# Performance work log

Measured on AMD Instinct MI355X. Metric: run time of the kernel, lower is better.

The kernel has to match this reference:

```python
import jax, jax.numpy as jnp
import numpy as np

EPS = 1e-7  # tf.keras.backend.epsilon()
DEGREE = 5
SCALE_BASE = 1.0
SCALE_LEGENDRE = 1.0


def legendre_basis(x, degree):
    # min/max normalization over the feature axis -> x_norm in [-1, 1]
    x_min = jnp.min(x, axis=-1, keepdims=True)
    x_max = jnp.max(x, axis=-1, keepdims=True)
    x_norm = 2.0 * (x - x_min) / (x_max - x_min + EPS) - 1.0
    polys = [jnp.ones_like(x_norm), x_norm]
    for n in range(2, degree + 1):
        p_n = ((2 * n - 1) * x_norm * polys[-1] - (n - 1) * polys[-2]) / n
        polys.append(p_n)
    return jnp.stack(polys, axis=-1)  # [b, i, degree+1]


def setup_inputs() -> dict:
    key = jax.random.key(0)
    k1, k2, k3 = jax.random.split(key, 3)
    b, i, o, d = 4096, 1024, 1024, DEGREE + 1
    x = jax.random.normal(k1, (b, i), dtype=jnp.float32)
    # HeUniform: limit = sqrt(6 / fan_in)
    lim_b = np.sqrt(6.0 / i)
    base_weight = jax.random.uniform(k2, (i, o), dtype=jnp.float32, minval=-lim_b, maxval=lim_b)
    legendre_weight = jax.random.uniform(k3, (i, o, d), dtype=jnp.float32, minval=-lim_b, maxval=lim_b)
    return {"x": x, "base_weight": base_weight, "legendre_weight": legendre_weight}


def reference(x, base_weight, legendre_weight):
    base_output = jax.nn.silu(x @ base_weight)  # [b, o]
    basis = legendre_basis(x, DEGREE)  # [b, i, d]
    # 'bi,iod,bid->bo' == fold x into the basis then contract (i, d)
    xb = x[..., None] * basis  # [b, i, d]
    legendre_output = jnp.einsum('bid,iod->bo', xb, legendre_weight)
    return SCALE_BASE * base_output + SCALE_LEGENDRE * legendre_output
```

## Files before the change

### kernel.cpp

```cpp
#include <hip/hip_runtime.h>
#include <stdint.h>

typedef unsigned short u16;
typedef unsigned int   u32;
typedef __attribute__((ext_vector_type(8)))  short bhalf8;
typedef __attribute__((ext_vector_type(16))) float f32x16;

#define B_ROWS 4096
#define I_DIM  1024
#define O_DIM  1024
#define N_D    6
#define K_LEG  (I_DIM * N_D)

#define BM 256
#define BN 256
#define BK 64
#define NS 28
#define BUF_BYTES 65536
#define LDS_BYTES 131072

__device__ __forceinline__ u16 f2b(float f) {
  u32 u = __float_as_uint(f);
  return (u16)((u + 0x7fffu + ((u >> 16) & 1u)) >> 16);
}

__device__ __forceinline__ void gld_lds16(const void* g, void* l) {
  __builtin_amdgcn_global_load_lds(
      (const __attribute__((address_space(1))) u32*)(uintptr_t)g,
      (__attribute__((address_space(3))) u32*)(u32)(uintptr_t)l, 16, 0, 0);
}

#define RS 201
__global__ void k_prep(const float* __restrict__ bw, const float* __restrict__ lw,
                       const float* __restrict__ x,
                       u16* __restrict__ Bb, u16* __restrict__ Bl,
                       u16* __restrict__ Ab, u16* __restrict__ Al) {
  __shared__ float t[32 * RS];
  if (blockIdx.x < 1024) {
    const int bx = blockIdx.x & 31, by = blockIdx.x >> 5;
    const int i0 = by * 32, o0 = bx * 32;
    const int c = threadIdx.x & 31, r0 = threadIdx.x >> 5;
    #pragma unroll
    for (int k = 0; k < 4; ++k) {
      int r = r0 + k * 8;
      t[r * 33 + c] = bw[(size_t)(i0 + r) * O_DIM + o0 + c];
    }
    __syncthreads();
    #pragma unroll
    for (int k = 0; k < 4; ++k) {
      int r = r0 + k * 8;
      Bb[(size_t)(o0 + r) * I_DIM + i0 + c] = f2b(t[c * 33 + r]);
    }
  } else if (blockIdx.x < 2048) {
    const int blk = blockIdx.x - 1024;
    const int bx = blk & 31, by = blk >> 5;
    const int i0 = by * 32, o0 = bx * 32;
    for (int q = threadIdx.x; q < 32 * 48; q += 256) {
      int ri = q / 48, s4 = q % 48;
      float4 v = *(const float4*)(lw + (size_t)(i0 + ri) * (O_DIM * N_D) + o0 * N_D + s4 * 4);
      float* p = t + ri * RS + s4 * 4;
      p[0] = v.x; p[1] = v.y; p[2] = v.z; p[3] = v.w;
    }
    __syncthreads();
    for (int q = threadIdx.x; q < 32 * 96; q += 256) {
      int ro = q / 96, k = q % 96;
      int e0 = 2 * k, e1 = 2 * k + 1;
      float v0 = t[(e0 / 6) * RS + ro * 6 + (e0 % 6)];
      float v1 = t[(e1 / 6) * RS + ro * 6 + (e1 % 6)];
      u32* dst = (u32*)(Bl + (size_t)(o0 + ro) * K_LEG + i0 * N_D);
      dst[k] = (u32)f2b(v0) | ((u32)f2b(v1) << 16);
    }
  } else {
    const int b = blockIdx.x - 2048;
    const int tt = threadIdx.x;
    float4 v = ((const float4*)(x + (size_t)b * I_DIM))[tt];
    float mn = fminf(fminf(v.x, v.y), fminf(v.z, v.w));
    float mx = fmaxf(fmaxf(v.x, v.y), fmaxf(v.z, v.w));
    #pragma unroll
    for (int off = 32; off > 0; off >>= 1) {
      mn = fminf(mn, __shfl_xor(mn, off, 64));
      mx = fmaxf(mx, __shfl_xor(mx, off, 64));
    }
    __shared__ float smn[4], smx[4];
    if ((tt & 63) == 0) { smn[tt >> 6] = mn; smx[tt >> 6] = mx; }
    __syncthreads();
    mn = fminf(fminf(smn[0], smn[1]), fminf(smn[2], smn[3]));
    mx = fmaxf(fmaxf(smx[0], smx[1]), fmaxf(smx[2], smx[3]));
    float sc = 2.0f / (mx - mn + 1e-7f);

    float xs[4] = {v.x, v.y, v.z, v.w};
    u32 lb[12];
    #pragma unroll
    for (int e = 0; e < 4; ++e) {
      float xv = xs[e];
      float xn = (xv - mn) * sc - 1.0f;
      float p0 = 1.0f, p1 = xn;
      float p2 = (3.0f * xn * p1 - 1.0f * p0) * (1.0f / 2.0f);
      float p3 = (5.0f * xn * p2 - 2.0f * p1) * (1.0f / 3.0f);
      float p4 = (7.0f * xn * p3 - 3.0f * p2) * (1.0f / 4.0f);
      float p5 = (9.0f * xn * p4 - 4.0f * p3) * (1.0f / 5.0f);
      lb[e * 3 + 0] = (u32)f2b(xv * p0) | ((u32)f2b(xv * p1) << 16);
      lb[e * 3 + 1] = (u32)f2b(xv * p2) | ((u32)f2b(xv * p3) << 16);
      lb[e * 3 + 2] = (u32)f2b(xv * p4) | ((u32)f2b(xv * p5) << 16);
    }
    u32 a0 = (u32)f2b(xs[0]) | ((u32)f2b(xs[1]) << 16);
    u32 a1 = (u32)f2b(xs[2]) | ((u32)f2b(xs[3]) << 16);
    *(uint2*)(Ab + (size_t)b * I_DIM + tt * 4) = make_uint2(a0, a1);
    uint4* dl = (uint4*)(Al + (size_t)b * K_LEG + tt * 24);
    dl[0] = make_uint4(lb[0], lb[1], lb[2], lb[3]);
    dl[1] = make_uint4(lb[4], lb[5], lb[6], lb[7]);
    dl[2] = make_uint4(lb[8], lb[9], lb[10], lb[11]);
  }
}

__global__ __launch_bounds__(512, 2) void k_gemm(
    const u16* __restrict__ Ab, const u16* __restrict__ Bb,
    const u16* __restrict__ Al, const u16* __restrict__ Bl,
    float* __restrict__ out, float* __restrict__ P) {
  extern __shared__ char lds[];

  const int tid  = threadIdx.x;
  const int wave = tid >> 6;
  const int lane = tid & 63;
  const int wm = wave >> 2;
  const int wn = wave & 3;
  const u32 lr = (u32)lane & 31;
  const u32 hi = (u32)lane >> 5;

  const int bid   = blockIdx.x;
  const int bx    = bid >> 4;
  const int by    = (bid >> 2) & 3;
  const int split = bid & 3;
  const size_t brow = (size_t)bx * BM;
  const size_t bcol = (size_t)by * BN;
  const bool s0 = (split == 0);
  const int legbase = s0 ? 0 : (12 + 28 * (split - 1));

  const int rt = tid >> 3;
  const u32 ct = (((u32)tid & 7) ^ ((u32)rt & 7)) * 8;

  auto stage_half = [&](int v, int h) {
    char* dst = lds + (size_t)(v & 1) * BUF_BYTES + ((h >= 2) ? 32768 : 0)
              + (size_t)(h & 1) * 16384 + (size_t)tid * 16;
    const size_t rbase = ((h < 2) ? brow : bcol) + (size_t)(h & 1) * 128 + (size_t)rt;
    const u16* src0;
    size_t rstep;
    if (s0 && v < 16) {
      const u16* M = (h < 2) ? Ab : Bb;
      src0 = M + rbase * I_DIM + (size_t)v * BK + ct;
      rstep = (size_t)64 * I_DIM;
    } else {
      const int lv = s0 ? (v - 16) : (legbase + v);
      const u16* M = (h < 2) ? Al : Bl;
      src0 = M + rbase * K_LEG + (size_t)lv * BK + ct;
      rstep = (size_t)64 * K_LEG;
    }
    gld_lds16(src0, dst);
    gld_lds16(src0 + rstep, dst + 8192);
  };

  const u32 c0off = (hi ^ ((u32)lane & 7)) * 16;
  const u32 abase = ((u32)wm * 128 + lr) * 128;
  const u32 bbase = 32768u + ((u32)wn * 64 + lr) * 128;

  f32x16 acc[4][2] = {};
  bhalf8 afa[4], bfa[2], afb[4], bfb[2];

#define READF(AF, BF, P_, KK) do {                                            \
    const u32 co_ = c0off ^ ((KK) << 5);                                      \
    BF[0] = *(const bhalf8*)((P_) + bbase + co_);                             \
    BF[1] = *(const bhalf8*)((P_) + bbase + 4096 + co_);                      \
    AF[0] = *(const bhalf8*)((P_) + abase + co_);                             \
    AF[1] = *(const bhalf8*)((P_) + abase + 4096 + co_);                      \
    AF[2] = *(const bhalf8*)((P_) + abase + 8192 + co_);                      \
    AF[3] = *(const bhalf8*)((P_) + abase + 12288 + co_);                     \
  } while (0)

#define MM(AF, BF) do {                                                       \
    __builtin_amdgcn_s_setprio(1);                                            \
    _Pragma("unroll")                                                         \
    for (int m = 0; m < 4; ++m)                                               \
      _Pragma("unroll")                                                       \
      for (int n = 0; n < 2; ++n)                                             \
        acc[m][n] = __builtin_amdgcn_mfma_f32_32x32x16_bf16(AF[m], BF[n], acc[m][n], 0, 0, 0); \
    __builtin_amdgcn_s_setprio(0);                                            \
  } while (0)

  stage_half(0, 0); stage_half(0, 1); stage_half(0, 2); stage_half(0, 3);
  __syncthreads();

  for (int u = 0; u < NS; ++u) {
    if (s0 && u == 16) {
      #pragma unroll
      for (int m = 0; m < 4; ++m)
        #pragma unroll
        for (int n = 0; n < 2; ++n)
          #pragma unroll
          for (int j = 0; j < 16; ++j) {
            float v = acc[m][n][j];
            acc[m][n][j] = v / (1.0f + __expf(-v));
          }
    }
    const char* p = lds + (size_t)(u & 1) * BUF_BYTES;
    const bool st = (u < NS - 1);
    READF(afa, bfa, p, 0);
    if (st) stage_half(u + 1, 0);
    READF(afb, bfb, p, 1);
    MM(afa, bfa);
    if (st) stage_half(u + 1, 1);
    READF(afa, bfa, p, 2);
    MM(afb, bfb);
    if (st) stage_half(u + 1, 2);
    READF(afb, bfb, p, 3);
    MM(afa, bfa);
    if (st) stage_half(u + 1, 3);
    MM(afb, bfb);
    __syncthreads();
  }
#undef READF
#undef MM

  float* dst = s0 ? out : (P + (size_t)(split - 1) * ((size_t)B_ROWS * O_DIM));
  #pragma unroll
  for (int m = 0; m < 4; ++m)
    #pragma unroll
    for (int n = 0; n < 2; ++n) {
      const size_t rb = brow + wm * 128 + m * 32 + 4 * hi;
      const size_t c  = bcol + wn * 64 + n * 32 + lr;
      #pragma unroll
      for (int j = 0; j < 16; ++j) {
        const size_t r = rb + (j & 3) + 8 * (j >> 2);
        dst[r * O_DIM + c] = acc[m][n][j];
      }
    }
}

__global__ void k_reduce(float* __restrict__ out, const float* __restrict__ P) {
  const size_t i = (size_t)blockIdx.x * 256 + threadIdx.x;
  const size_t NE = (size_t)B_ROWS * O_DIM / 4;
  float4 a = ((const float4*)out)[i];
  float4 b = ((const float4*)P)[i];
  float4 c = ((const float4*)P)[i + NE];
  float4 d = ((const float4*)P)[i + 2 * NE];
  a.x += b.x + c.x + d.x;  a.y += b.y + c.y + d.y;
  a.z += b.z + c.z + d.z;  a.w += b.w + c.w + d.w;
  ((float4*)out)[i] = a;
}

extern "C" void kernel_launch(void* const* d_in, const int* in_sizes, int n_in,
                              void* d_out, int out_size, void* d_ws, size_t ws_size,
                              hipStream_t stream) {
  const float* x  = (const float*)d_in[0];
  const float* bw = (const float*)d_in[1];
  const float* lw = (const float*)d_in[2];
  float* out = (float*)d_out;

  char* w = (char*)d_ws;
  u16*  Ab = (u16*)(w);
  u16*  Al = (u16*)(w + (size_t)8   * 1024 * 1024);
  u16*  Bb = (u16*)(w + (size_t)56  * 1024 * 1024);
  u16*  Bl = (u16*)(w + (size_t)58  * 1024 * 1024);
  float* P = (float*)(w + (size_t)72 * 1024 * 1024);

  hipFuncSetAttribute((const void*)k_gemm,
                      hipFuncAttributeMaxDynamicSharedMemorySize, LDS_BYTES);

  k_prep  <<<dim3(2048 + B_ROWS), 256, 0, stream>>>(bw, lw, x, Bb, Bl, Ab, Al);
  k_gemm  <<<dim3(4 * (B_ROWS / BM) * (O_DIM / BN)), 512, LDS_BYTES, stream>>>(Ab, Bb, Al, Bl, out, P);
  k_reduce<<<dim3((B_ROWS * O_DIM / 4) / 256), 256, 0, stream>>>(out, P);
}
```

Before: 108.5 us.

## Shrink GEMM tile to 128x128 with 2-way split-K and simplify reduction

Changes the fused GEMM block tile from 256x256 with 512 threads and 4-way split-K to 128x128 with 256 threads and 2-way split-K, doubling K steps per block. The staging uses incrementing global pointers and an explicit vmcnt wait plus barrier, and the reduce kernel now adds only one partial buffer. This cuts partial-sum traffic and the reduction cost, but it halves per-block operand reuse, raising global and L2 load volume per FLOP, and lengthens each block's serial K loop.

```diff
diff --git a/kernel.cpp b/kernel.cpp
--- a/kernel.cpp
+++ b/kernel.cpp
@@ -12,12 +12,12 @@
 #define N_D    6
 #define K_LEG  (I_DIM * N_D)
 
-#define BM 256
-#define BN 256
+#define BM 128
+#define BN 128
 #define BK 64
-#define NS 28
-#define BUF_BYTES 65536
-#define LDS_BYTES 131072
+#define NS 56
+#define BUF_BYTES 32768
+#define LDS_BYTES 65536
 
 __device__ __forceinline__ u16 f2b(float f) {
   u32 u = __float_as_uint(f);
@@ -113,7 +113,7 @@
   }
 }
 
-__global__ __launch_bounds__(512, 2) void k_gemm(
+__global__ __launch_bounds__(256, 2) void k_gemm(
     const u16* __restrict__ Ab, const u16* __restrict__ Bb,
     const u16* __restrict__ Al, const u16* __restrict__ Bl,
     float* __restrict__ out, float* __restrict__ P) {
@@ -122,49 +122,48 @@
   const int tid  = threadIdx.x;
   const int wave = tid >> 6;
   const int lane = tid & 63;
-  const int wm = wave >> 2;
-  const int wn = wave & 3;
+  const int wm = wave >> 1;
+  const int wn = wave & 1;
   const u32 lr = (u32)lane & 31;
   const u32 hi = (u32)lane >> 5;
 
   const int bid   = blockIdx.x;
   const int bx    = bid >> 4;
-  const int by    = (bid >> 2) & 3;
-  const int split = bid & 3;
+  const int by    = (bid >> 1) & 7;
+  const int split = bid & 1;
   const size_t brow = (size_t)bx * BM;
   const size_t bcol = (size_t)by * BN;
   const bool s0 = (split == 0);
-  const int legbase = s0 ? 0 : (12 + 28 * (split - 1));
+  const int legbase = s0 ? 0 : 40;
 
   const int rt = tid >> 3;
   const u32 ct = (((u32)tid & 7) ^ ((u32)rt & 7)) * 8;
 
-  auto stage_half = [&](int v, int h) {
-    char* dst = lds + (size_t)(v & 1) * BUF_BYTES + ((h >= 2) ? 32768 : 0)
-              + (size_t)(h & 1) * 16384 + (size_t)tid * 16;
-    const size_t rbase = ((h < 2) ? brow : bcol) + (size_t)(h & 1) * 128 + (size_t)rt;
-    const u16* src0;
-    size_t rstep;
-    if (s0 && v < 16) {
-      const u16* M = (h < 2) ? Ab : Bb;
-      src0 = M + rbase * I_DIM + (size_t)v * BK + ct;
-      rstep = (size_t)64 * I_DIM;
-    } else {
-      const int lv = s0 ? (v - 16) : (legbase + v);
-      const u16* M = (h < 2) ? Al : Bl;
-      src0 = M + rbase * K_LEG + (size_t)lv * BK + ct;
-      rstep = (size_t)64 * K_LEG;
-    }
-    gld_lds16(src0, dst);
-    gld_lds16(src0 + rstep, dst + 8192);
+  const u16 *gA, *gB;
+  size_t ldk, ldk32;
+  auto set_ptrs = [&](const u16* A, const u16* Bt, size_t ldk_, size_t kt) {
+    ldk = ldk_; ldk32 = 32 * ldk_;
+    gA = A  + (brow + rt) * ldk_ + kt * BK + ct;
+    gB = Bt + (bcol + rt) * ldk_ + kt * BK + ct;
   };
+  if (s0) set_ptrs(Ab, Bb, I_DIM, 0);
+  else    set_ptrs(Al, Bl, K_LEG, (size_t)legbase);
+
+  auto stg = [&](int v, int h) {
+    if (s0 && v == 16 && h == 0) set_ptrs(Al, Bl, K_LEG, 0);
+    char* dst = lds + (size_t)(v & 1) * BUF_BYTES + ((h >= 4) ? 16384 : 0)
+              + (size_t)(h & 3) * 4096 + (size_t)tid * 16;
+    const u16* src = ((h < 4) ? gA : gB) + (size_t)(h & 3) * ldk32;
+    gld_lds16(src, dst);
+    if (h == 7) { gA += BK; gB += BK; }
+  };
 
   const u32 c0off = (hi ^ ((u32)lane & 7)) * 16;
-  const u32 abase = ((u32)wm * 128 + lr) * 128;
-  const u32 bbase = 32768u + ((u32)wn * 64 + lr) * 128;
-
-  f32x16 acc[4][2] = {};
-  bhalf8 afa[4], bfa[2], afb[4], bfb[2];
+  const u32 abase = ((u32)wm * 64 + lr) * 128;
+  const u32 bbase = 16384u + ((u32)wn * 64 + lr) * 128;
+
+  f32x16 acc[2][2] = {};
+  bhalf8 fa0[2], fb0[2], fa1[2], fb1[2], fa2[2], fb2[2], fa3[2], fb3[2];
 
 #define READF(AF, BF, P_, KK) do {                                            \
     const u32 co_ = c0off ^ ((KK) << 5);                                      \
@@ -172,27 +171,26 @@
     BF[1] = *(const bhalf8*)((P_) + bbase + 4096 + co_);                      \
     AF[0] = *(const bhalf8*)((P_) + abase + co_);                             \
     AF[1] = *(const bhalf8*)((P_) + abase + 4096 + co_);                      \
-    AF[2] = *(const bhalf8*)((P_) + abase + 8192 + co_);                      \
-    AF[3] = *(const bhalf8*)((P_) + abase + 12288 + co_);                     \
   } while (0)
 
 #define MM(AF, BF) do {                                                       \
     __builtin_amdgcn_s_setprio(1);                                            \
     _Pragma("unroll")                                                         \
-    for (int m = 0; m < 4; ++m)                                               \
+    for (int m = 0; m < 2; ++m)                                               \
       _Pragma("unroll")                                                       \
       for (int n = 0; n < 2; ++n)                                             \
         acc[m][n] = __builtin_amdgcn_mfma_f32_32x32x16_bf16(AF[m], BF[n], acc[m][n], 0, 0, 0); \
     __builtin_amdgcn_s_setprio(0);                                            \
   } while (0)
 
-  stage_half(0, 0); stage_half(0, 1); stage_half(0, 2); stage_half(0, 3);
+  #pragma unroll
+  for (int h = 0; h < 8; ++h) stg(0, h);
   __syncthreads();
 
   for (int u = 0; u < NS; ++u) {
     if (s0 && u == 16) {
       #pragma unroll
-      for (int m = 0; m < 4; ++m)
+      for (int m = 0; m < 2; ++m)
         #pragma unroll
         for (int n = 0; n < 2; ++n)
           #pragma unroll
@@ -203,29 +201,31 @@
     }
     const char* p = lds + (size_t)(u & 1) * BUF_BYTES;
     const bool st = (u < NS - 1);
-    READF(afa, bfa, p, 0);
-    if (st) stage_half(u + 1, 0);
-    READF(afb, bfb, p, 1);
-    MM(afa, bfa);
-    if (st) stage_half(u + 1, 1);
-    READF(afa, bfa, p, 2);
-    MM(afb, bfb);
-    if (st) stage_half(u + 1, 2);
-    READF(afb, bfb, p, 3);
-    MM(afa, bfa);
-    if (st) stage_half(u + 1, 3);
-    MM(afb, bfb);
-    __syncthreads();
+    READF(fa0, fb0, p, 0);
+    if (st) { stg(u + 1, 0); stg(u + 1, 1); }
+    READF(fa1, fb1, p, 1);
+    MM(fa0, fb0);
+    if (st) { stg(u + 1, 2); stg(u + 1, 3); }
+    READF(fa2, fb2, p, 2);
+    MM(fa1, fb1);
+    if (st) { stg(u + 1, 4); stg(u + 1, 5); }
+    READF(fa3, fb3, p, 3);
+    MM(fa2, fb2);
+    if (st) { stg(u + 1, 6); stg(u + 1, 7); }
+    MM(fa3, fb3);
+    asm volatile("s_waitcnt vmcnt(0)" ::: "memory");
+    __builtin_amdgcn_s_barrier();
+    __builtin_amdgcn_sched_barrier(0);
   }
 #undef READF
 #undef MM
 
-  float* dst = s0 ? out : (P + (size_t)(split - 1) * ((size_t)B_ROWS * O_DIM));
+  float* dst = s0 ? out : P;
   #pragma unroll
-  for (int m = 0; m < 4; ++m)
+  for (int m = 0; m < 2; ++m)
     #pragma unroll
     for (int n = 0; n < 2; ++n) {
-      const size_t rb = brow + wm * 128 + m * 32 + 4 * hi;
+      const size_t rb = brow + wm * 64 + m * 32 + 4 * hi;
       const size_t c  = bcol + wn * 64 + n * 32 + lr;
       #pragma unroll
       for (int j = 0; j < 16; ++j) {
@@ -237,13 +237,9 @@
 
 __global__ void k_reduce(float* __restrict__ out, const float* __restrict__ P) {
   const size_t i = (size_t)blockIdx.x * 256 + threadIdx.x;
-  const size_t NE = (size_t)B_ROWS * O_DIM / 4;
   float4 a = ((const float4*)out)[i];
   float4 b = ((const float4*)P)[i];
-  float4 c = ((const float4*)P)[i + NE];
-  float4 d = ((const float4*)P)[i + 2 * NE];
-  a.x += b.x + c.x + d.x;  a.y += b.y + c.y + d.y;
-  a.z += b.z + c.z + d.z;  a.w += b.w + c.w + d.w;
+  a.x += b.x;  a.y += b.y;  a.z += b.z;  a.w += b.w;
   ((float4*)out)[i] = a;
 }
 
@@ -266,6 +262,6 @@
                       hipFuncAttributeMaxDynamicSharedMemorySize, LDS_BYTES);
 
   k_prep  <<<dim3(2048 + B_ROWS), 256, 0, stream>>>(bw, lw, x, Bb, Bl, Ab, Al);
-  k_gemm  <<<dim3(4 * (B_ROWS / BM) * (O_DIM / BN)), 512, LDS_BYTES, stream>>>(Ab, Bb, Al, Bl, out, P);
+  k_gemm  <<<dim3(2 * (B_ROWS / BM) * (O_DIM / BN)), 256, LDS_BYTES, stream>>>(Ab, Bb, Al, Bl, out, P);
   k_reduce<<<dim3((B_ROWS * O_DIM / 4) / 256), 256, 0, stream>>>(out, P);
 }
```

New measurement: 107.4 us. No clear change (-1.0%).

## Switch GEMM to 16x16x32 MFMA with 4-phase pipelined staging and bf16 split-K partials

Applied to the files above, without the earlier changes.

Rewrites the main GEMM loop to use 16x16x32 bf16 MFMAs with a new LDS layout and swizzle. Global-to-LDS loads are issued two stages ahead, and each iteration is split into four phases with explicit vmcnt/lgkmcnt waits, barriers and sched_barriers, so loads overlap with compute. Split-K partial sums are now stored as bf16 instead of fp32, which halves partial-buffer traffic in the gemm and reduce kernels. The cost is lower precision in the partials and fragile hand-tuned wait counts.

```diff
diff --git a/kernel.cpp b/kernel.cpp
--- a/kernel.cpp
+++ b/kernel.cpp
@@ -3,8 +3,8 @@
 
 typedef unsigned short u16;
 typedef unsigned int   u32;
-typedef __attribute__((ext_vector_type(8)))  short bhalf8;
-typedef __attribute__((ext_vector_type(16))) float f32x16;
+typedef __attribute__((ext_vector_type(8))) short bhalf8;
+typedef __attribute__((ext_vector_type(4))) float f32x4;
 
 #define B_ROWS 4096
 #define I_DIM  1024
@@ -12,16 +12,15 @@
 #define N_D    6
 #define K_LEG  (I_DIM * N_D)
 
-#define BM 256
-#define BN 256
-#define BK 64
-#define NS 28
-#define BUF_BYTES 65536
+#define NU 28
 #define LDS_BYTES 131072
 
 __device__ __forceinline__ u16 f2b(float f) {
   u32 u = __float_as_uint(f);
   return (u16)((u + 0x7fffu + ((u >> 16) & 1u)) >> 16);
+}
+__device__ __forceinline__ float b2f(u16 h) {
+  return __uint_as_float((u32)h << 16);
 }
 
 __device__ __forceinline__ void gld_lds16(const void* g, void* l) {
@@ -116,7 +115,7 @@
 __global__ __launch_bounds__(512, 2) void k_gemm(
     const u16* __restrict__ Ab, const u16* __restrict__ Bb,
     const u16* __restrict__ Al, const u16* __restrict__ Bl,
-    float* __restrict__ out, float* __restrict__ P) {
+    float* __restrict__ out, u16* __restrict__ Pb) {
   extern __shared__ char lds[];
 
   const int tid  = threadIdx.x;
@@ -124,126 +123,159 @@
   const int lane = tid & 63;
   const int wm = wave >> 2;
   const int wn = wave & 3;
-  const u32 lr = (u32)lane & 31;
-  const u32 hi = (u32)lane >> 5;
+  const u32 l15 = (u32)lane & 15;
 
   const int bid   = blockIdx.x;
   const int bx    = bid >> 4;
   const int by    = (bid >> 2) & 3;
   const int split = bid & 3;
-  const size_t brow = (size_t)bx * BM;
-  const size_t bcol = (size_t)by * BN;
+  const size_t brow = (size_t)bx * 256;
+  const size_t bcol = (size_t)by * 256;
   const bool s0 = (split == 0);
   const int legbase = s0 ? 0 : (12 + 28 * (split - 1));
 
-  const int rt = tid >> 3;
-  const u32 ct = (((u32)tid & 7) ^ ((u32)rt & 7)) * 8;
-
-  auto stage_half = [&](int v, int h) {
-    char* dst = lds + (size_t)(v & 1) * BUF_BYTES + ((h >= 2) ? 32768 : 0)
-              + (size_t)(h & 1) * 16384 + (size_t)tid * 16;
-    const size_t rbase = ((h < 2) ? brow : bcol) + (size_t)(h & 1) * 128 + (size_t)rt;
-    const u16* src0;
-    size_t rstep;
-    if (s0 && v < 16) {
-      const u16* M = (h < 2) ? Ab : Bb;
-      src0 = M + rbase * I_DIM + (size_t)v * BK + ct;
-      rstep = (size_t)64 * I_DIM;
-    } else {
-      const int lv = s0 ? (v - 16) : (legbase + v);
-      const u16* M = (h < 2) ? Al : Bl;
-      src0 = M + rbase * K_LEG + (size_t)lv * BK + ct;
-      rstep = (size_t)64 * K_LEG;
-    }
-    gld_lds16(src0, dst);
-    gld_lds16(src0 + rstep, dst + 8192);
+  const int rS = tid >> 2;
+  const u32 cS = (((u32)tid & 3) ^ (((u32)rS >> 1) & 3)) * 8;
+
+  auto stage = [&](int v, int h) {
+    const int isB = h & 1, kkh = h >> 1;
+    char* dst = lds + ((v & 1) * 65536 + isB * 32768 + kkh * 16384) + (size_t)tid * 16;
+    const u16* M; size_t ldk; int kt;
+    if (s0 && v < 16) { M = isB ? Bb : Ab; ldk = I_DIM; kt = v; }
+    else { M = isB ? Bl : Al; ldk = K_LEG; kt = s0 ? (v - 16) : (legbase + v); }
+    const u16* src = M + ((isB ? bcol : brow) + (size_t)rS) * ldk
+                   + (size_t)kt * 64 + kkh * 32 + cS;
+    gld_lds16(src, dst);
+    gld_lds16(src + 128 * ldk, dst + 8192);
   };
 
-  const u32 c0off = (hi ^ ((u32)lane & 7)) * 16;
-  const u32 abase = ((u32)wm * 128 + lr) * 128;
-  const u32 bbase = 32768u + ((u32)wn * 64 + lr) * 128;
-
-  f32x16 acc[4][2] = {};
-  bhalf8 afa[4], bfa[2], afb[4], bfb[2];
-
-#define READF(AF, BF, P_, KK) do {                                            \
-    const u32 co_ = c0off ^ ((KK) << 5);                                      \
-    BF[0] = *(const bhalf8*)((P_) + bbase + co_);                             \
-    BF[1] = *(const bhalf8*)((P_) + bbase + 4096 + co_);                      \
-    AF[0] = *(const bhalf8*)((P_) + abase + co_);                             \
-    AF[1] = *(const bhalf8*)((P_) + abase + 4096 + co_);                      \
-    AF[2] = *(const bhalf8*)((P_) + abase + 8192 + co_);                      \
-    AF[3] = *(const bhalf8*)((P_) + abase + 12288 + co_);                     \
-  } while (0)
-
-#define MM(AF, BF) do {                                                       \
+  const u32 chnk = ((((u32)lane >> 4) & 3) ^ ((l15 >> 1) & 3)) * 16;
+  const u32 aoff = ((u32)wm * 128 + l15) * 64 + chnk;
+  const u32 boff = 32768u + ((u32)wn * 64 + l15) * 64 + chnk;
+
+  f32x4 acc[8][4] = {};
+  bhalf8 Aev[8], Aod[8], Bn01[2], Bn23[2];
+
+  auto silu = [&]() {
+    #pragma unroll
+    for (int m = 0; m < 8; ++m)
+      #pragma unroll
+      for (int n = 0; n < 4; ++n)
+        #pragma unroll
+        for (int j = 0; j < 4; ++j) {
+          float v = acc[m][n][j];
+          acc[m][n][j] = v / (1.0f + __expf(-v));
+        }
+  };
+
+#define SB   __builtin_amdgcn_sched_barrier(0)
+#define BARR __builtin_amdgcn_s_barrier()
+#define VMW(N) asm volatile("s_waitcnt vmcnt(" #N ")" ::: "memory")
+#define RD_A(SET, DB, KKH) do { const char* q_ = lds + (DB) + (KKH)*16384 + aoff; \
+    SET[0]=*(const bhalf8*)(q_);      SET[1]=*(const bhalf8*)(q_+1024);       \
+    SET[2]=*(const bhalf8*)(q_+2048); SET[3]=*(const bhalf8*)(q_+3072);       \
+    SET[4]=*(const bhalf8*)(q_+4096); SET[5]=*(const bhalf8*)(q_+5120);       \
+    SET[6]=*(const bhalf8*)(q_+6144); SET[7]=*(const bhalf8*)(q_+7168); } while(0)
+#define RD_B01(DB, KKH) do { const char* q_ = lds + (DB) + (KKH)*16384 + boff; \
+    Bn01[0]=*(const bhalf8*)(q_);      Bn01[1]=*(const bhalf8*)(q_+1024); } while(0)
+#define RD_B23(DB, KKH) do { const char* q_ = lds + (DB) + (KKH)*16384 + boff; \
+    Bn23[0]=*(const bhalf8*)(q_+2048); Bn23[1]=*(const bhalf8*)(q_+3072); } while(0)
+#define MFMA8(ASET, B0_, B1_, NB) do {                                        \
     __builtin_amdgcn_s_setprio(1);                                            \
     _Pragma("unroll")                                                         \
-    for (int m = 0; m < 4; ++m)                                               \
-      _Pragma("unroll")                                                       \
-      for (int n = 0; n < 2; ++n)                                             \
-        acc[m][n] = __builtin_amdgcn_mfma_f32_32x32x16_bf16(AF[m], BF[n], acc[m][n], 0, 0, 0); \
+    for (int m_ = 0; m_ < 8; ++m_) {                                          \
+      acc[m_][NB]   = __builtin_amdgcn_mfma_f32_16x16x32_bf16(ASET[m_], B0_, acc[m_][NB],   0,0,0); \
+      acc[m_][NB+1] = __builtin_amdgcn_mfma_f32_16x16x32_bf16(ASET[m_], B1_, acc[m_][NB+1], 0,0,0); \
+    }                                                                         \
     __builtin_amdgcn_s_setprio(0);                                            \
-  } while (0)
-
-  stage_half(0, 0); stage_half(0, 1); stage_half(0, 2); stage_half(0, 3);
-  __syncthreads();
-
-  for (int u = 0; u < NS; ++u) {
-    if (s0 && u == 16) {
+  } while(0)
+
+#define PH1(DB, STG, WT) do { RD_B23(DB, 0); STG; SB; WT; BARR;               \
+    asm volatile("s_waitcnt lgkmcnt(2)" ::: "memory"); SB;                    \
+    MFMA8(Aev, Bn01[0], Bn01[1], 0); BARR; } while(0)
+#define PH2(DB, STG, WT) do { RD_A(Aod, DB, 1); RD_B01(DB, 1); STG; SB; WT; BARR; \
+    asm volatile("s_waitcnt lgkmcnt(10)" ::: "memory"); SB;                   \
+    MFMA8(Aev, Bn23[0], Bn23[1], 2); BARR; } while(0)
+#define PH3(DB, STG, WT) do { RD_B23(DB, 1); STG; SB; WT; BARR;               \
+    asm volatile("s_waitcnt lgkmcnt(2)" ::: "memory"); SB;                    \
+    MFMA8(Aod, Bn01[0], Bn01[1], 0); BARR; } while(0)
+#define PH4(DB2, STG) do { RD_A(Aev, DB2, 0); RD_B01(DB2, 0); STG; SB; BARR;  \
+    asm volatile("s_waitcnt lgkmcnt(10)" ::: "memory"); SB;                   \
+    MFMA8(Aod, Bn23[0], Bn23[1], 2); BARR; } while(0)
+#define PH4LAST() do {                                                        \
+    asm volatile("s_waitcnt lgkmcnt(0)" ::: "memory"); SB;                    \
+    MFMA8(Aod, Bn23[0], Bn23[1], 2); } while(0)
+
+  stage(0, 0); stage(0, 1); stage(0, 2); stage(0, 3);
+  stage(1, 0); stage(1, 1); stage(1, 2);
+  VMW(6); BARR;
+  RD_A(Aev, 0u, 0); RD_B01(0u, 0);
+
+  for (int u = 0; u < NU - 2; ++u) {
+    if (s0 && u == 16) silu();
+    const u32 db  = (u & 1) ? 65536u : 0u;
+    const u32 db2 = 65536u - db;
+    PH1(db, stage(u + 1, 3), VMW(10));
+    PH2(db, stage(u + 2, 0), VMW(10));
+    PH3(db, stage(u + 2, 1), VMW(8));
+    PH4(db2, stage(u + 2, 2));
+  }
+  PH1(0u, stage(27, 3), VMW(10));
+  PH2(0u, (void)0, VMW(8));
+  PH3(0u, (void)0, VMW(4));
+  PH4(65536u, (void)0);
+  PH1(65536u, (void)0, VMW(2));
+  PH2(65536u, (void)0, VMW(0));
+  PH3(65536u, (void)0, (void)0);
+  PH4LAST();
+
+#undef PH1
+#undef PH2
+#undef PH3
+#undef PH4
+#undef PH4LAST
+#undef MFMA8
+#undef RD_A
+#undef RD_B01
+#undef RD_B23
+
+  if (s0) {
+    #pragma unroll
+    for (int m = 0; m < 8; ++m)
       #pragma unroll
-      for (int m = 0; m < 4; ++m)
+      for (int n = 0; n < 4; ++n) {
+        const size_t r0 = brow + wm * 128 + m * 16 + (lane >> 4) * 4;
+        const size_t c  = bcol + wn * 64 + n * 16 + l15;
         #pragma unroll
-        for (int n = 0; n < 2; ++n)
-          #pragma unroll
-          for (int j = 0; j < 16; ++j) {
-            float v = acc[m][n][j];
-            acc[m][n][j] = v / (1.0f + __expf(-v));
-          }
-    }
-    const char* p = lds + (size_t)(u & 1) * BUF_BYTES;
-    const bool st = (u < NS - 1);
-    READF(afa, bfa, p, 0);
-    if (st) stage_half(u + 1, 0);
-    READF(afb, bfb, p, 1);
-    MM(afa, bfa);
-    if (st) stage_half(u + 1, 1);
-    READF(afa, bfa, p, 2);
-    MM(afb, bfb);
-    if (st) stage_half(u + 1, 2);
-    READF(afb, bfb, p, 3);
-    MM(afa, bfa);
-    if (st) stage_half(u + 1, 3);
-    MM(afb, bfb);
-    __syncthreads();
+        for (int j = 0; j < 4; ++j)
+          out[(r0 + j) * O_DIM + c] = acc[m][n][j];
+      }
+  } else {
+    u16* dst = Pb + (size_t)(split - 1) * ((size_t)B_ROWS * O_DIM);
+    #pragma unroll
+    for (int m = 0; m < 8; ++m)
+      #pragma unroll
+      for (int n = 0; n < 4; ++n) {
+        const size_t r0 = brow + wm * 128 + m * 16 + (lane >> 4) * 4;
+        const size_t c  = bcol + wn * 64 + n * 16 + l15;
+        #pragma unroll
+        for (int j = 0; j < 4; ++j)
+          dst[(r0 + j) * O_DIM + c] = f2b(acc[m][n][j]);
+      }
   }
-#undef READF
-#undef MM
-
-  float* dst = s0 ? out : (P + (size_t)(split - 1) * ((size_t)B_ROWS * O_DIM));
-  #pragma unroll
-  for (int m = 0; m < 4; ++m)
-    #pragma unroll
-    for (int n = 0; n < 2; ++n) {
-      const size_t rb = brow + wm * 128 + m * 32 + 4 * hi;
-      const size_t c  = bcol + wn * 64 + n * 32 + lr;
-      #pragma unroll
-      for (int j = 0; j < 16; ++j) {
-        const size_t r = rb + (j & 3) + 8 * (j >> 2);
-        dst[r * O_DIM + c] = acc[m][n][j];
-      }
-    }
-}
-
-__global__ void k_reduce(float* __restrict__ out, const float* __restrict__ P) {
+}
+
+__global__ void k_reduce(float* __restrict__ out, const u16* __restrict__ Pb) {
   const size_t i = (size_t)blockIdx.x * 256 + threadIdx.x;
-  const size_t NE = (size_t)B_ROWS * O_DIM / 4;
+  const size_t NE = (size_t)B_ROWS * O_DIM;
   float4 a = ((const float4*)out)[i];
-  float4 b = ((const float4*)P)[i];
-  float4 c = ((const float4*)P)[i + NE];
-  float4 d = ((const float4*)P)[i + 2 * NE];
-  a.x += b.x + c.x + d.x;  a.y += b.y + c.y + d.y;
-  a.z += b.z + c.z + d.z;  a.w += b.w + c.w + d.w;
+  ushort4 p0 = ((const ushort4*)Pb)[i];
+  ushort4 p1 = ((const ushort4*)(Pb + NE))[i];
+  ushort4 p2 = ((const ushort4*)(Pb + 2 * NE))[i];
+  a.x += b2f(p0.x) + b2f(p1.x) + b2f(p2.x);
+  a.y += b2f(p0.y) + b2f(p1.y) + b2f(p2.y);
+  a.z += b2f(p0.z) + b2f(p1.z) + b2f(p2.z);
+  a.w += b2f(p0.w) + b2f(p1.w) + b2f(p2.w);
   ((float4*)out)[i] = a;
 }
 
@@ -256,16 +288,16 @@
   float* out = (float*)d_out;
 
   char* w = (char*)d_ws;
-  u16*  Ab = (u16*)(w);
-  u16*  Al = (u16*)(w + (size_t)8   * 1024 * 1024);
-  u16*  Bb = (u16*)(w + (size_t)56  * 1024 * 1024);
-  u16*  Bl = (u16*)(w + (size_t)58  * 1024 * 1024);
-  float* P = (float*)(w + (size_t)72 * 1024 * 1024);
+  u16* Ab = (u16*)(w);
+  u16* Al = (u16*)(w + (size_t)8   * 1024 * 1024);
+  u16* Bb = (u16*)(w + (size_t)56  * 1024 * 1024);
+  u16* Bl = (u16*)(w + (size_t)58  * 1024 * 1024);
+  u16* Pb = (u16*)(w + (size_t)72  * 1024 * 1024);
 
   hipFuncSetAttribute((const void*)k_gemm,
                       hipFuncAttributeMaxDynamicSharedMemorySize, LDS_BYTES);
 
   k_prep  <<<dim3(2048 + B_ROWS), 256, 0, stream>>>(bw, lw, x, Bb, Bl, Ab, Al);
-  k_gemm  <<<dim3(4 * (B_ROWS / BM) * (O_DIM / BN)), 512, LDS_BYTES, stream>>>(Ab, Bb, Al, Bl, out, P);
-  k_reduce<<<dim3((B_ROWS * O_DIM / 4) / 256), 256, 0, stream>>>(out, P);
-}
+  k_gemm  <<<dim3(256), 512, LDS_BYTES, stream>>>(Ab, Bb, Al, Bl, out, Pb);
+  k_reduce<<<dim3((B_ROWS * O_DIM / 4) / 256), 256, 0, stream>>>(out, Pb);
+}
```

Measured after the change: 103.2 us. 1.05x faster.

## Store split-K partials as bf16 and restructure GEMM pipeline with staggered LDS reads

Applied to the files above, without the earlier changes.

Split-K partial results are now written as bf16 instead of fp32, halving partial write and reduce read traffic, with some accuracy loss in the partial sums. The main loop is rewritten into quarter steps with explicit lgkmcnt waits and sched_barriers around each MFMA batch. Waves in the two M halves read the K sub-chunks in a staggered order to spread LDS bank pressure. The loop now waits for vmcnt(0) plus a raw s_barrier instead of calling __syncthreads.

```diff
diff --git a/kernel.cpp b/kernel.cpp
--- a/kernel.cpp
+++ b/kernel.cpp
@@ -12,16 +12,15 @@
 #define N_D    6
 #define K_LEG  (I_DIM * N_D)
 
-#define BM 256
-#define BN 256
-#define BK 64
-#define NS 28
-#define BUF_BYTES 65536
+#define NU 28
 #define LDS_BYTES 131072
 
 __device__ __forceinline__ u16 f2b(float f) {
   u32 u = __float_as_uint(f);
   return (u16)((u + 0x7fffu + ((u >> 16) & 1u)) >> 16);
+}
+__device__ __forceinline__ float b2f(u16 h) {
+  return __uint_as_float((u32)h << 16);
 }
 
 __device__ __forceinline__ void gld_lds16(const void* g, void* l) {
@@ -116,7 +115,7 @@
 __global__ __launch_bounds__(512, 2) void k_gemm(
     const u16* __restrict__ Ab, const u16* __restrict__ Bb,
     const u16* __restrict__ Al, const u16* __restrict__ Bl,
-    float* __restrict__ out, float* __restrict__ P) {
+    float* __restrict__ out, u16* __restrict__ Pb) {
   extern __shared__ char lds[];
 
   const int tid  = threadIdx.x;
@@ -131,32 +130,22 @@
   const int bx    = bid >> 4;
   const int by    = (bid >> 2) & 3;
   const int split = bid & 3;
-  const size_t brow = (size_t)bx * BM;
-  const size_t bcol = (size_t)by * BN;
+  const size_t brow = (size_t)bx * 256;
+  const size_t bcol = (size_t)by * 256;
   const bool s0 = (split == 0);
   const int legbase = s0 ? 0 : (12 + 28 * (split - 1));
 
   const int rt = tid >> 3;
-  const u32 ct = (((u32)tid & 7) ^ ((u32)rt & 7)) * 8;
-
-  auto stage_half = [&](int v, int h) {
-    char* dst = lds + (size_t)(v & 1) * BUF_BYTES + ((h >= 2) ? 32768 : 0)
-              + (size_t)(h & 1) * 16384 + (size_t)tid * 16;
-    const size_t rbase = ((h < 2) ? brow : bcol) + (size_t)(h & 1) * 128 + (size_t)rt;
-    const u16* src0;
-    size_t rstep;
-    if (s0 && v < 16) {
-      const u16* M = (h < 2) ? Ab : Bb;
-      src0 = M + rbase * I_DIM + (size_t)v * BK + ct;
-      rstep = (size_t)64 * I_DIM;
-    } else {
-      const int lv = s0 ? (v - 16) : (legbase + v);
-      const u16* M = (h < 2) ? Al : Bl;
-      src0 = M + rbase * K_LEG + (size_t)lv * BK + ct;
-      rstep = (size_t)64 * K_LEG;
-    }
-    gld_lds16(src0, dst);
-    gld_lds16(src0 + rstep, dst + 8192);
+  const u32 ct8 = (((u32)tid & 7) ^ ((u32)rt & 7)) * 8;
+
+  auto stg = [&](int v, int h) {
+    char* dst = lds + (size_t)((v & 1) * 65536 + ((h & 4) << 13) + (h & 3) * 8192)
+              + (size_t)tid * 16;
+    const u16* M; size_t ldk; int kt;
+    if (s0 && v < 16) { M = (h & 4) ? Bb : Ab; ldk = I_DIM; kt = v; }
+    else { M = (h & 4) ? Bl : Al; ldk = K_LEG; kt = s0 ? (v - 16) : (legbase + v); }
+    const size_t r = ((h & 4) ? bcol : brow) + (size_t)((h & 3) * 64 + rt);
+    gld_lds16(M + r * ldk + (size_t)kt * 64 + ct8, dst);
   };
 
   const u32 c0off = (hi ^ ((u32)lane & 7)) * 16;
@@ -164,86 +153,118 @@
   const u32 bbase = 32768u + ((u32)wn * 64 + lr) * 128;
 
   f32x16 acc[4][2] = {};
-  bhalf8 afa[4], bfa[2], afb[4], bfb[2];
-
-#define READF(AF, BF, P_, KK) do {                                            \
-    const u32 co_ = c0off ^ ((KK) << 5);                                      \
-    BF[0] = *(const bhalf8*)((P_) + bbase + co_);                             \
-    BF[1] = *(const bhalf8*)((P_) + bbase + 4096 + co_);                      \
-    AF[0] = *(const bhalf8*)((P_) + abase + co_);                             \
-    AF[1] = *(const bhalf8*)((P_) + abase + 4096 + co_);                      \
-    AF[2] = *(const bhalf8*)((P_) + abase + 8192 + co_);                      \
-    AF[3] = *(const bhalf8*)((P_) + abase + 12288 + co_);                     \
+  bhalf8 Ae[4], Be[2], Ao[4], Bo[2];
+
+  auto silu = [&]() {
+    #pragma unroll
+    for (int m = 0; m < 4; ++m)
+      #pragma unroll
+      for (int n = 0; n < 2; ++n)
+        #pragma unroll
+        for (int j = 0; j < 16; ++j) {
+          float v = acc[m][n][j];
+          acc[m][n][j] = v / (1.0f + __expf(-v));
+        }
+  };
+
+#define RDQ(SA, SB_, P_, KK) do {                                             \
+    const u32 co_ = c0off ^ ((u32)(KK) << 5);                                 \
+    SB_[0] = *(const bhalf8*)((P_) + bbase + co_);                            \
+    SB_[1] = *(const bhalf8*)((P_) + bbase + 4096 + co_);                     \
+    SA[0]  = *(const bhalf8*)((P_) + abase + co_);                            \
+    SA[1]  = *(const bhalf8*)((P_) + abase + 4096 + co_);                     \
+    SA[2]  = *(const bhalf8*)((P_) + abase + 8192 + co_);                     \
+    SA[3]  = *(const bhalf8*)((P_) + abase + 12288 + co_);                    \
   } while (0)
 
-#define MM(AF, BF) do {                                                       \
+#define MM(SA, SB_) do {                                                      \
+    asm volatile("s_waitcnt lgkmcnt(0)" ::: "memory");                        \
+    __builtin_amdgcn_sched_barrier(0);                                        \
     __builtin_amdgcn_s_setprio(1);                                            \
     _Pragma("unroll")                                                         \
-    for (int m = 0; m < 4; ++m)                                               \
+    for (int m_ = 0; m_ < 4; ++m_)                                            \
       _Pragma("unroll")                                                       \
-      for (int n = 0; n < 2; ++n)                                             \
-        acc[m][n] = __builtin_amdgcn_mfma_f32_32x32x16_bf16(AF[m], BF[n], acc[m][n], 0, 0, 0); \
+      for (int n_ = 0; n_ < 2; ++n_)                                          \
+        acc[m_][n_] = __builtin_amdgcn_mfma_f32_32x32x16_bf16(SA[m_], SB_[n_], acc[m_][n_], 0, 0, 0); \
     __builtin_amdgcn_s_setprio(0);                                            \
+    __builtin_amdgcn_sched_barrier(0);                                        \
   } while (0)
 
-  stage_half(0, 0); stage_half(0, 1); stage_half(0, 2); stage_half(0, 3);
-  __syncthreads();
-
-  for (int u = 0; u < NS; ++u) {
-    if (s0 && u == 16) {
+#define QTR(KK, SA, SB_, H0) do {                                             \
+    RDQ(SA, SB_, p, KK);                                                      \
+    if (st) { stg(u + 1, H0); stg(u + 1, (H0) + 1); }                         \
+    MM(SA, SB_);                                                              \
+  } while (0)
+
+  #pragma unroll
+  for (int h = 0; h < 8; ++h) stg(0, h);
+  asm volatile("s_waitcnt vmcnt(0)" ::: "memory");
+  __builtin_amdgcn_s_barrier();
+
+  for (int u = 0; u < NU; ++u) {
+    if (s0 && u == 16) silu();
+    const char* p = lds + (size_t)(u & 1) * 65536;
+    const bool st = (u < NU - 1);
+    if (wm == 0) {
+      QTR(0, Ae, Be, 0);
+      QTR(1, Ao, Bo, 2);
+      QTR(2, Ae, Be, 4);
+      QTR(3, Ao, Bo, 6);
+    } else {
+      QTR(2, Ae, Be, 0);
+      QTR(3, Ao, Bo, 2);
+      QTR(0, Ae, Be, 4);
+      QTR(1, Ao, Bo, 6);
+    }
+    asm volatile("s_waitcnt vmcnt(0)" ::: "memory");
+    __builtin_amdgcn_s_barrier();
+    __builtin_amdgcn_sched_barrier(0);
+  }
+#undef QTR
+#undef MM
+#undef RDQ
+
+  if (s0) {
+    #pragma unroll
+    for (int m = 0; m < 4; ++m)
       #pragma unroll
-      for (int m = 0; m < 4; ++m)
+      for (int n = 0; n < 2; ++n) {
+        const size_t rb = brow + wm * 128 + m * 32 + 4 * hi;
+        const size_t c  = bcol + wn * 64 + n * 32 + lr;
         #pragma unroll
-        for (int n = 0; n < 2; ++n)
-          #pragma unroll
-          for (int j = 0; j < 16; ++j) {
-            float v = acc[m][n][j];
-            acc[m][n][j] = v / (1.0f + __expf(-v));
-          }
-    }
-    const char* p = lds + (size_t)(u & 1) * BUF_BYTES;
-    const bool st = (u < NS - 1);
-    READF(afa, bfa, p, 0);
-    if (st) stage_half(u + 1, 0);
-    READF(afb, bfb, p, 1);
-    MM(afa, bfa);
-    if (st) stage_half(u + 1, 1);
-    READF(afa, bfa, p, 2);
-    MM(afb, bfb);
-    if (st) stage_half(u + 1, 2);
-    READF(afb, bfb, p, 3);
-    MM(afa, bfa);
-    if (st) stage_half(u + 1, 3);
-    MM(afb, bfb);
-    __syncthreads();
+        for (int j = 0; j < 16; ++j) {
+          const size_t r = rb + (j & 3) + 8 * (j >> 2);
+          out[r * O_DIM + c] = acc[m][n][j];
+        }
+      }
+  } else {
+    u16* dst = Pb + (size_t)(split - 1) * ((size_t)B_ROWS * O_DIM);
+    #pragma unroll
+    for (int m = 0; m < 4; ++m)
+      #pragma unroll
+      for (int n = 0; n < 2; ++n) {
+        const size_t rb = brow + wm * 128 + m * 32 + 4 * hi;
+        const size_t c  = bcol + wn * 64 + n * 32 + lr;
+        #pragma unroll
+        for (int j = 0; j < 16; ++j) {
+          const size_t r = rb + (j & 3) + 8 * (j >> 2);
+          dst[r * O_DIM + c] = f2b(acc[m][n][j]);
+        }
+      }
   }
-#undef READF
-#undef MM
-
-  float* dst = s0 ? out : (P + (size_t)(split - 1) * ((size_t)B_ROWS * O_DIM));
-  #pragma unroll
-  for (int m = 0; m < 4; ++m)
-    #pragma unroll
-    for (int n = 0; n < 2; ++n) {
-      const size_t rb = brow + wm * 128 + m * 32 + 4 * hi;
-      const size_t c  = bcol + wn * 64 + n * 32 + lr;
-      #pragma unroll
-      for (int j = 0; j < 16; ++j) {
-        const size_t r = rb + (j & 3) + 8 * (j >> 2);
-        dst[r * O_DIM + c] = acc[m][n][j];
-      }
-    }
-}
-
-__global__ void k_reduce(float* __restrict__ out, const float* __restrict__ P) {
+}
+
+__global__ void k_reduce(float* __restrict__ out, const u16* __restrict__ Pb) {
   const size_t i = (size_t)blockIdx.x * 256 + threadIdx.x;
-  const size_t NE = (size_t)B_ROWS * O_DIM / 4;
+  const size_t NE = (size_t)B_ROWS * O_DIM;
   float4 a = ((const float4*)out)[i];
-  float4 b = ((const float4*)P)[i];
-  float4 c = ((const float4*)P)[i + NE];
-  float4 d = ((const float4*)P)[i + 2 * NE];
-  a.x += b.x + c.x + d.x;  a.y += b.y + c.y + d.y;
-  a.z += b.z + c.z + d.z;  a.w += b.w + c.w + d.w;
+  ushort4 p0 = ((const ushort4*)Pb)[i];
+  ushort4 p1 = ((const ushort4*)(Pb + NE))[i];
+  ushort4 p2 = ((const ushort4*)(Pb + 2 * NE))[i];
+  a.x += b2f(p0.x) + b2f(p1.x) + b2f(p2.x);
+  a.y += b2f(p0.y) + b2f(p1.y) + b2f(p2.y);
+  a.z += b2f(p0.z) + b2f(p1.z) + b2f(p2.z);
+  a.w += b2f(p0.w) + b2f(p1.w) + b2f(p2.w);
   ((float4*)out)[i] = a;
 }
 
@@ -256,16 +277,16 @@
   float* out = (float*)d_out;
 
   char* w = (char*)d_ws;
-  u16*  Ab = (u16*)(w);
-  u16*  Al = (u16*)(w + (size_t)8   * 1024 * 1024);
-  u16*  Bb = (u16*)(w + (size_t)56  * 1024 * 1024);
-  u16*  Bl = (u16*)(w + (size_t)58  * 1024 * 1024);
-  float* P = (float*)(w + (size_t)72 * 1024 * 1024);
+  u16* Ab = (u16*)(w);
+  u16* Al = (u16*)(w + (size_t)8   * 1024 * 1024);
+  u16* Bb = (u16*)(w + (size_t)56  * 1024 * 1024);
+  u16* Bl = (u16*)(w + (size_t)58  * 1024 * 1024);
+  u16* Pb = (u16*)(w + (size_t)72  * 1024 * 1024);
 
   hipFuncSetAttribute((const void*)k_gemm,
                       hipFuncAttributeMaxDynamicSharedMemorySize, LDS_BYTES);
 
   k_prep  <<<dim3(2048 + B_ROWS), 256, 0, stream>>>(bw, lw, x, Bb, Bl, Ab, Al);
-  k_gemm  <<<dim3(4 * (B_ROWS / BM) * (O_DIM / BN)), 512, LDS_BYTES, stream>>>(Ab, Bb, Al, Bl, out, P);
-  k_reduce<<<dim3((B_ROWS * O_DIM / 4) / 256), 256, 0, stream>>>(out, P);
-}
+  k_gemm  <<<dim3(256), 512, LDS_BYTES, stream>>>(Ab, Bb, Al, Bl, out, Pb);
+  k_reduce<<<dim3((B_ROWS * O_DIM / 4) / 256), 256, 0, stream>>>(out, Pb);
+}
```

Result: no change. 108.1 us (-0.3%).
